# Kernel optimization log

Measured on AMD Instinct MI355X. Metric: run time of the kernel, lower is better.

The kernel has to match this reference:

```python
import jax, jax.numpy as jnp
import numpy as np

B = 16384
F = 1024
DELTA = 0.3
LAMB = 0.0005


def setup_inputs() -> dict:
    key = jax.random.key(0)
    k1, k2, k3, k4 = jax.random.split(key, 4)
    skt = jax.random.normal(k1, (B, F), dtype=jnp.float32)
    imgp = jax.random.normal(k2, (B, F), dtype=jnp.float32)
    imgn = jax.random.normal(k3, (B, F), dtype=jnp.float32)
    eye = jnp.eye(F, dtype=jnp.float32)
    w = eye + 0.05 * jax.random.normal(k4, (F, F), dtype=jnp.float32)
    return {"skt": skt, "imgp": imgp, "imgn": imgn, "w": w, "eye": eye}


def _distance(v1, v2, w, w_rowsum, w_colsum):
    # sum_{i,j} w[i,j] * (v1[:,i] - v2[:,j])**2
    #   = (v1**2) @ w.sum(1) - 2 * v1 @ w @ v2^T (diag) + (v2**2) @ w.sum(0)
    cross = ((v1 @ w) * v2).sum(axis=-1)  # [B]
    return (v1 * v1) @ w_rowsum - 2.0 * cross + (v2 * v2) @ w_colsum


def reference(skt, imgp, imgn, w, eye):
    w_rowsum = w.sum(axis=1)  # [F]
    w_colsum = w.sum(axis=0)  # [F]
    dp = _distance(skt, imgp, w, w_rowsum, w_colsum)  # [B]
    dn = _distance(skt, imgn, w, w_rowsum, w_colsum)  # [B]
    hinge = jnp.maximum(DELTA + dp - dn, 0.0).mean()
    dw = w - eye
    regu = jnp.abs(dw).sum() + jnp.sqrt((dw * dw).sum())
    return hinge + LAMB * regu
```

## Files before the change

kernel.cpp:

```cpp
#include <hip/hip_runtime.h>
#include <hip/hip_bf16.h>

#define FDIM 1024
#define BROWS 16384
#define DELTA_C 0.3f
#define LAMB_C 0.0005f

typedef __bf16 bf8v __attribute__((ext_vector_type(8)));
typedef float f4v __attribute__((ext_vector_type(4)));
typedef unsigned short u16;
typedef u16 u16x8 __attribute__((ext_vector_type(8)));

#define WS_PABS_OFF 4160
#define WS_PSQ_OFF 4672
#define WS_ROWACC_OFF 8192
#define WS_WB_OFF 131072
#define WS_SKTB_OFF (131072 + (1u << 21))
#define WS_NEED_FULL ((size_t)WS_SKTB_OFF + ((size_t)1 << 25))

__device__ __forceinline__ u16 f2bf(float f) {
  unsigned u = __builtin_bit_cast(unsigned, f);
  u += 0x7fffu + ((u >> 16) & 1u);
  return (u16)(u >> 16);
}

__device__ __forceinline__ void gload_lds16(const void* g, void* l) {
  __builtin_amdgcn_global_load_lds(
      (const __attribute__((address_space(1))) unsigned int*)g,
      (__attribute__((address_space(3))) unsigned int*)l, 16, 0, 0);
}

template <bool DO_A>
__global__ __launch_bounds__(256) void prep_all(const float* __restrict__ w,
                                                const float* __restrict__ skt,
                                                float* __restrict__ colsum,
                                                float* __restrict__ pabs,
                                                float* __restrict__ psq,
                                                u16* __restrict__ wb,
                                                u16* __restrict__ sktb) {
  __shared__ char smem_u[17440];
  const int t = threadIdx.x;
  const int bid = blockIdx.x;

  if (bid < 128) {
    u16(*tile)[1024] = (u16(*)[1024])smem_u;
    float* red = (float*)(smem_u + 16384);
    const int b = bid;
    const int k0 = b * 8;
    const int col = t * 4;

    float cs0 = 0.f, cs1 = 0.f, cs2 = 0.f, cs3 = 0.f;
    float aacc = 0.f, sacc = 0.f;
#pragma unroll
    for (int i = 0; i < 8; ++i) {
      const int gk = k0 + i;
      const float4 v = *(const float4*)(w + (size_t)gk * FDIM + col);
      ushort4 bb;
      bb.x = f2bf(v.x); bb.y = f2bf(v.y); bb.z = f2bf(v.z); bb.w = f2bf(v.w);
      *(ushort4*)(&tile[i][col]) = bb;
      cs0 += v.x; cs1 += v.y; cs2 += v.z; cs3 += v.w;
      const float d0 = v.x - (gk == col + 0 ? 1.f : 0.f);
      const float d1 = v.y - (gk == col + 1 ? 1.f : 0.f);
      const float d2 = v.z - (gk == col + 2 ? 1.f : 0.f);
      const float d3 = v.w - (gk == col + 3 ? 1.f : 0.f);
      aacc += fabsf(d0) + fabsf(d1) + fabsf(d2) + fabsf(d3);
      sacc += d0 * d0 + d1 * d1 + d2 * d2 + d3 * d3;
    }
    atomicAdd(&colsum[col + 0], cs0);
    atomicAdd(&colsum[col + 1], cs1);
    atomicAdd(&colsum[col + 2], cs2);
    atomicAdd(&colsum[col + 3], cs3);
#pragma unroll
    for (int off = 1; off < 64; off <<= 1) {
      aacc += __shfl_xor(aacc, off);
      sacc += __shfl_xor(sacc, off);
    }
    const int wid = t >> 6;
    if ((t & 63) == 0) { red[wid] = aacc; red[4 + wid] = sacc; }
    __syncthreads();
    if (t == 0) pabs[b] = red[0] + red[1] + red[2] + red[3];
    if (t == 1) psq[b] = red[4] + red[5] + red[6] + red[7];
#pragma unroll
    for (int j = 0; j < 4; ++j) {
      const int n = col + j;
      u16x8 pk;
#pragma unroll
      for (int e = 0; e < 8; ++e) pk[e] = tile[e][n];
      *(u16x8*)(wb + ((size_t)b * FDIM + n) * 8) = pk;
    }
  } else if constexpr (DO_A) {
    u16(*tile)[136] = (u16(*)[136])smem_u;
    const int ab = bid - 128;
    const int mb = ab >> 3;
    const int kb = ab & 7;
    const int m0 = mb * 64, k0 = kb * 128;
#pragma unroll
    for (int i = 0; i < 8; ++i) {
      const int fid = i * 256 + t;
      const int ml = fid >> 5;
      const int c4 = fid & 31;
      const float4 v = *(const float4*)(skt + (size_t)(m0 + ml) * FDIM + k0 + c4 * 4);
      ushort4 b;
      b.x = f2bf(v.x); b.y = f2bf(v.y); b.z = f2bf(v.z); b.w = f2bf(v.w);
      *(ushort4*)(&tile[ml][c4 * 4]) = b;
    }
    __syncthreads();
    const int ks0 = k0 >> 3;
#pragma unroll
    for (int i = 0; i < 4; ++i) {
      const int uid = i * 256 + t;
      const int si = uid >> 6;
      const int ml = uid & 63;
      const u16x8 pk = *(const u16x8*)(&tile[ml][si * 8]);
      *(u16x8*)(sktb + ((size_t)(ks0 + si) * BROWS + m0 + ml) * 8) = pk;
    }
  }
}

template <bool PRE>
__global__ __launch_bounds__(512, 4) void hofel_main(
    const float* __restrict__ skt, const float* __restrict__ imgp,
    const float* __restrict__ imgn, const u16* __restrict__ wb,
    const u16* __restrict__ sktb, const float* __restrict__ colsum,
    float* __restrict__ rowacc) {
  __shared__ u16 ldsT[3][12288];
  __shared__ float lds_cs[128];

  const int t = threadIdx.x;
  const int lane = t & 63;
  const int wid = t >> 6;
  const int l15 = lane & 15;
  const int l4 = lane >> 4;

  const int swz = (blockIdx.x & 7) * 64 + (blockIdx.x >> 3);
  const int mt = swz >> 3, nt = swz & 7;
  const int m0 = mt * 256, n0 = nt * 128;

  const int wr = wid >> 1, wc = wid & 1;
  const int wm = wr * 64, wn = wc * 64;

  f4v acc[4][4];
#pragma unroll
  for (int mi = 0; mi < 4; ++mi)
#pragma unroll
    for (int ni = 0; ni < 4; ++ni) {
      f4v z = {0.f, 0.f, 0.f, 0.f};
      acc[mi][ni] = z;
    }

  auto stage = [&](int buf, int kt) {
#pragma unroll
    for (int r = 0; r < 2; ++r) {
      const int o = r * 8192 + wid * 1024;
      const int ol = o + lane * 16;
      const int s = ol >> 12;
      const int m = (ol >> 4) & 255;
      gload_lds16((const char*)(sktb + ((size_t)(kt * 4 + s) * BROWS + m0 + m) * 8),
                  (char*)ldsT[buf] + o);
    }
    {
      const int o2 = wid * 1024;
      const int ol2 = o2 + lane * 16;
      const int s = ol2 >> 11;
      const int n = (ol2 >> 4) & 127;
      gload_lds16((const char*)(wb + ((size_t)(kt * 4 + s) * FDIM + n0 + n) * 8),
                  (char*)ldsT[buf] + 16384 + o2);
    }
  };

  auto compute_tile = [&](int buf) {
    const char* bufb = (const char*)ldsT[buf];
    bf8v aF[4], bF[4];
#pragma unroll
    for (int mi = 0; mi < 4; ++mi)
      aF[mi] = *(const bf8v*)(bufb + l4 * 4096 + (wm + mi * 16 + l15) * 16);
#pragma unroll
    for (int ni = 0; ni < 4; ++ni)
      bF[ni] = *(const bf8v*)(bufb + 16384 + l4 * 2048 + (wn + ni * 16 + l15) * 16);
#pragma unroll
    for (int mi = 0; mi < 4; ++mi)
#pragma unroll
      for (int ni = 0; ni < 4; ++ni)
        acc[mi][ni] = __builtin_amdgcn_mfma_f32_16x16x32_bf16(aF[mi], bF[ni], acc[mi][ni], 0, 0, 0);
  };

  if constexpr (PRE) {
    if (t < 128) lds_cs[t] = colsum[n0 + t];
    asm volatile("s_waitcnt vmcnt(0) lgkmcnt(0)" ::: "memory");
    __builtin_amdgcn_sched_barrier(0);
    stage(0, 0);
    stage(1, 1);
    asm volatile("s_waitcnt vmcnt(3)" ::: "memory");
    __builtin_amdgcn_s_barrier();
    __builtin_amdgcn_sched_barrier(0);

    int cur = 0;
    for (int kt = 0; kt < 32; ++kt) {
      if (kt + 2 < 32) {
        const int nb = (cur >= 1) ? cur - 1 : cur + 2;
        stage(nb, kt + 2);
      }
      compute_tile(cur);
      if (kt < 30) {
        asm volatile("s_waitcnt vmcnt(3)" ::: "memory");
        __builtin_amdgcn_s_barrier();
        __builtin_amdgcn_sched_barrier(0);
      } else if (kt == 30) {
        asm volatile("s_waitcnt vmcnt(0)" ::: "memory");
        __builtin_amdgcn_s_barrier();
        __builtin_amdgcn_sched_barrier(0);
      }
      cur = (cur == 2) ? 0 : cur + 1;
    }
  } else {
    if (t < 128) lds_cs[t] = colsum[n0 + t];
    for (int kt = 0; kt < 32; ++kt) {
      __syncthreads();
      {
        const int o2 = wid * 1024;
        const int ol2 = o2 + lane * 16;
        const int s = ol2 >> 11;
        const int n = (ol2 >> 4) & 127;
        gload_lds16((const char*)(wb + ((size_t)(kt * 4 + s) * FDIM + n0 + n) * 8),
                    (char*)ldsT[0] + 16384 + o2);
      }
      const int m = t >> 1, h = t & 1;
      const float* ap = skt + (size_t)(m0 + m) * FDIM + kt * 32 + h * 16;
#pragma unroll
      for (int q = 0; q < 2; ++q) {
        const float4 v0 = *(const float4*)(ap + q * 8);
        const float4 v1 = *(const float4*)(ap + q * 8 + 4);
        u16x8 pk;
        pk[0] = f2bf(v0.x); pk[1] = f2bf(v0.y); pk[2] = f2bf(v0.z); pk[3] = f2bf(v0.w);
        pk[4] = f2bf(v1.x); pk[5] = f2bf(v1.y); pk[6] = f2bf(v1.z); pk[7] = f2bf(v1.w);
        *(u16x8*)((char*)ldsT[0] + (h * 2 + q) * 4096 + m * 16) = pk;
      }
      __syncthreads();
      compute_tile(0);
    }
  }

#pragma unroll
  for (int mi = 0; mi < 4; ++mi) {
#pragma unroll
    for (int rr = 0; rr < 4; ++rr) {
      const int row = m0 + wm + mi * 16 + l4 * 4 + rr;
      const float* pr = imgp + (size_t)row * FDIM + n0;
      const float* nr = imgn + (size_t)row * FDIM + n0;
      float s = 0.f;
#pragma unroll
      for (int ni = 0; ni < 4; ++ni) {
        const int cl = wn + ni * 16 + l15;
        const float T = acc[mi][ni][rr];
        const float p = pr[cl];
        const float q = nr[cl];
        s += (p - q) * (-2.f * T + (p + q) * lds_cs[cl]);
      }
#pragma unroll
      for (int off = 1; off < 16; off <<= 1) s += __shfl_xor(s, off);
      if (l15 == 0) atomicAdd(rowacc + row, s);
    }
  }
}

__global__ __launch_bounds__(1024) void hinge_reduce(const float* __restrict__ rowacc,
                                                     float* __restrict__ wsf) {
  __shared__ float part[16];
  const int t = threadIdx.x;
  const int id = blockIdx.x * 1024 + t;
  float v = fmaxf(DELTA_C + rowacc[id], 0.f);
#pragma unroll
  for (int off = 1; off < 64; off <<= 1) v += __shfl_xor(v, off);
  if ((t & 63) == 0) part[t >> 6] = v;
  __syncthreads();
  if (t < 16) {
    float x = part[t];
#pragma unroll
    for (int off = 1; off < 16; off <<= 1) x += __shfl_xor(x, off);
    if (t == 0) atomicAdd(&wsf[0], x);
  }
}

__global__ __launch_bounds__(128) void finalize_k(const float* __restrict__ wsf,
                                                  const float* __restrict__ pabs,
                                                  const float* __restrict__ psq,
                                                  float* __restrict__ out) {
  __shared__ float ra[2], rs[2];
  const int t = threadIdx.x;
  float a = pabs[t], s = psq[t];
#pragma unroll
  for (int off = 1; off < 64; off <<= 1) {
    a += __shfl_xor(a, off);
    s += __shfl_xor(s, off);
  }
  if ((t & 63) == 0) { ra[t >> 6] = a; rs[t >> 6] = s; }
  __syncthreads();
  if (t == 0)
    out[0] = wsf[0] * (1.f / (float)BROWS) +
             LAMB_C * ((ra[0] + ra[1]) + sqrtf(rs[0] + rs[1]));
}

extern "C" void kernel_launch(void* const* d_in, const int* in_sizes, int n_in,
                              void* d_out, int out_size, void* d_ws, size_t ws_size,
                              hipStream_t stream) {
  const float* skt  = (const float*)d_in[0];
  const float* imgp = (const float*)d_in[1];
  const float* imgn = (const float*)d_in[2];
  const float* w    = (const float*)d_in[3];

  float* wsf = (float*)d_ws;
  float* colsum = wsf + 16;
  float* pabs = (float*)((char*)d_ws + WS_PABS_OFF);
  float* psq = (float*)((char*)d_ws + WS_PSQ_OFF);
  float* rowacc = (float*)((char*)d_ws + WS_ROWACC_OFF);
  u16* wb = (u16*)((char*)d_ws + WS_WB_OFF);
  u16* sktb = (u16*)((char*)d_ws + WS_SKTB_OFF);
  float* out = (float*)d_out;

  hipMemsetAsync(d_ws, 0, WS_ROWACC_OFF + BROWS * sizeof(float), stream);

  if (ws_size >= WS_NEED_FULL) {
    prep_all<true><<<128 + 2048, 256, 0, stream>>>(w, skt, colsum, pabs, psq, wb, sktb);
    hofel_main<true><<<512, 512, 0, stream>>>(skt, imgp, imgn, wb, sktb, colsum, rowacc);
  } else {
    prep_all<false><<<128, 256, 0, stream>>>(w, skt, colsum, pabs, psq, wb, sktb);
    hofel_main<false><<<512, 512, 0, stream>>>(skt, imgp, imgn, wb, sktb, colsum, rowacc);
  }

  hinge_reduce<<<16, 1024, 0, stream>>>(rowacc, wsf);
  finalize_k<<<1, 128, 0, stream>>>(wsf, pabs, psq, out);
}
```

Before: 88.48 us.

## Enlarge GEMM tiles to 256x256 with 4-stage LDS pipeline and priority hints

Each block of the main GEMM now computes a 256x256 output tile instead of 256x128, so the grid halves to 256 blocks, one per CU. Each wave now holds a 128x64 accumulator. The LDS pipeline goes from three to four stages with three loads in flight. The compute is split into two MFMA half-phases around a barrier, wrapped in s_setprio to favour the matrix cores. The skt conversion blocks in the prep kernel are reordered by swizzle. The aim is more data reuse per staged byte and less LDS/global traffic per FLOP, at the cost of higher register pressure (launch bounds lowered to 2) and less occupancy to hide latency.

```diff
diff --git a/kernel.cpp b/kernel.cpp
--- a/kernel.cpp
+++ b/kernel.cpp
@@ -90,7 +90,8 @@
     }
   } else if constexpr (DO_A) {
     u16(*tile)[136] = (u16(*)[136])smem_u;
-    const int ab = bid - 128;
+    const int bidp = bid - 128;
+    const int ab = ((bidp & 7) << 8) | (bidp >> 3);
     const int mb = ab >> 3;
     const int kb = ab & 7;
     const int m0 = mb * 64, k0 = kb * 128;
@@ -117,14 +118,17 @@
   }
 }
 
+#define MM(mi, ni, a, b) \
+  acc[mi][ni] = __builtin_amdgcn_mfma_f32_16x16x32_bf16(a, b, acc[mi][ni], 0, 0, 0)
+
 template <bool PRE>
-__global__ __launch_bounds__(512, 4) void hofel_main(
+__global__ __launch_bounds__(512, 2) void hofel_main(
     const float* __restrict__ skt, const float* __restrict__ imgp,
     const float* __restrict__ imgn, const u16* __restrict__ wb,
     const u16* __restrict__ sktb, const float* __restrict__ colsum,
     float* __restrict__ rowacc) {
-  __shared__ u16 ldsT[3][12288];
-  __shared__ float lds_cs[128];
+  __shared__ u16 ldsT[4][16384];
+  __shared__ float lds_cs[256];
 
   const int t = threadIdx.x;
   const int lane = t & 63;
@@ -132,16 +136,19 @@
   const int l15 = lane & 15;
   const int l4 = lane >> 4;
 
-  const int swz = (blockIdx.x & 7) * 64 + (blockIdx.x >> 3);
-  const int mt = swz >> 3, nt = swz & 7;
-  const int m0 = mt * 256, n0 = nt * 128;
-
-  const int wr = wid >> 1, wc = wid & 1;
-  const int wm = wr * 64, wn = wc * 64;
-
-  f4v acc[4][4];
-#pragma unroll
-  for (int mi = 0; mi < 4; ++mi)
+  const int swz = (blockIdx.x & 7) * 32 + (blockIdx.x >> 3);
+  const int mt = swz >> 2, nt = swz & 3;
+  const int m0 = mt * 256, n0 = nt * 256;
+
+  const int wr = wid >> 2, wc = wid & 3;
+  const int wm = wr * 128, wn = wc * 64;
+
+  const int aoff = l4 * 4096 + (wm + l15) * 16;
+  const int boff = l4 * 4096 + (wn + l15) * 16;
+
+  f4v acc[8][4];
+#pragma unroll
+  for (int mi = 0; mi < 8; ++mi)
 #pragma unroll
     for (int ni = 0; ni < 4; ++ni) {
       f4v z = {0.f, 0.f, 0.f, 0.f};
@@ -158,71 +165,87 @@
       gload_lds16((const char*)(sktb + ((size_t)(kt * 4 + s) * BROWS + m0 + m) * 8),
                   (char*)ldsT[buf] + o);
     }
-    {
-      const int o2 = wid * 1024;
-      const int ol2 = o2 + lane * 16;
-      const int s = ol2 >> 11;
-      const int n = (ol2 >> 4) & 127;
+#pragma unroll
+    for (int r = 0; r < 2; ++r) {
+      const int o = r * 8192 + wid * 1024;
+      const int ol = o + lane * 16;
+      const int s = ol >> 12;
+      const int n = (ol >> 4) & 255;
       gload_lds16((const char*)(wb + ((size_t)(kt * 4 + s) * FDIM + n0 + n) * 8),
-                  (char*)ldsT[buf] + 16384 + o2);
+                  (char*)ldsT[buf] + 16384 + o);
     }
   };
 
-  auto compute_tile = [&](int buf) {
-    const char* bufb = (const char*)ldsT[buf];
-    bf8v aF[4], bF[4];
-#pragma unroll
-    for (int mi = 0; mi < 4; ++mi)
-      aF[mi] = *(const bf8v*)(bufb + l4 * 4096 + (wm + mi * 16 + l15) * 16);
-#pragma unroll
-    for (int ni = 0; ni < 4; ++ni)
-      bF[ni] = *(const bf8v*)(bufb + 16384 + l4 * 2048 + (wn + ni * 16 + l15) * 16);
-#pragma unroll
-    for (int mi = 0; mi < 4; ++mi)
-#pragma unroll
-      for (int ni = 0; ni < 4; ++ni)
-        acc[mi][ni] = __builtin_amdgcn_mfma_f32_16x16x32_bf16(aF[mi], bF[ni], acc[mi][ni], 0, 0, 0);
-  };
-
   if constexpr (PRE) {
-    if (t < 128) lds_cs[t] = colsum[n0 + t];
+    if (t < 256) lds_cs[t] = colsum[n0 + t];
     asm volatile("s_waitcnt vmcnt(0) lgkmcnt(0)" ::: "memory");
     __builtin_amdgcn_sched_barrier(0);
     stage(0, 0);
     stage(1, 1);
-    asm volatile("s_waitcnt vmcnt(3)" ::: "memory");
+    stage(2, 2);
+    asm volatile("s_waitcnt vmcnt(8)" ::: "memory");
     __builtin_amdgcn_s_barrier();
     __builtin_amdgcn_sched_barrier(0);
 
-    int cur = 0;
     for (int kt = 0; kt < 32; ++kt) {
-      if (kt + 2 < 32) {
-        const int nb = (cur >= 1) ? cur - 1 : cur + 2;
-        stage(nb, kt + 2);
-      }
-      compute_tile(cur);
-      if (kt < 30) {
-        asm volatile("s_waitcnt vmcnt(3)" ::: "memory");
-        __builtin_amdgcn_s_barrier();
-        __builtin_amdgcn_sched_barrier(0);
+      const char* ldsA = (const char*)ldsT[kt & 3];
+      const char* ldsB = ldsA + 16384;
+
+      bf8v bF0 = *(const bf8v*)(ldsB + boff);
+      bf8v bF1 = *(const bf8v*)(ldsB + boff + 256);
+      bf8v bF2 = *(const bf8v*)(ldsB + boff + 512);
+      bf8v bF3 = *(const bf8v*)(ldsB + boff + 768);
+      bf8v a0 = *(const bf8v*)(ldsA + aoff);
+      bf8v a1 = *(const bf8v*)(ldsA + aoff + 256);
+      bf8v a2 = *(const bf8v*)(ldsA + aoff + 512);
+      bf8v a3 = *(const bf8v*)(ldsA + aoff + 768);
+      if (kt < 29) stage((kt + 3) & 3, kt + 3);
+      asm volatile("s_waitcnt lgkmcnt(0)" ::: "memory");
+      __builtin_amdgcn_sched_barrier(0);
+      __builtin_amdgcn_s_setprio(1);
+      MM(0, 0, a0, bF0); MM(0, 1, a0, bF1); MM(0, 2, a0, bF2); MM(0, 3, a0, bF3);
+      MM(1, 0, a1, bF0); MM(1, 1, a1, bF1); MM(1, 2, a1, bF2); MM(1, 3, a1, bF3);
+      MM(2, 0, a2, bF0); MM(2, 1, a2, bF1); MM(2, 2, a2, bF2); MM(2, 3, a2, bF3);
+      MM(3, 0, a3, bF0); MM(3, 1, a3, bF1); MM(3, 2, a3, bF2); MM(3, 3, a3, bF3);
+      __builtin_amdgcn_s_setprio(0);
+      __builtin_amdgcn_s_barrier();
+      __builtin_amdgcn_sched_barrier(0);
+
+      a0 = *(const bf8v*)(ldsA + aoff + 1024);
+      a1 = *(const bf8v*)(ldsA + aoff + 1280);
+      a2 = *(const bf8v*)(ldsA + aoff + 1536);
+      a3 = *(const bf8v*)(ldsA + aoff + 1792);
+      asm volatile("s_waitcnt lgkmcnt(0)" ::: "memory");
+      __builtin_amdgcn_sched_barrier(0);
+      __builtin_amdgcn_s_setprio(1);
+      MM(4, 0, a0, bF0); MM(4, 1, a0, bF1); MM(4, 2, a0, bF2); MM(4, 3, a0, bF3);
+      MM(5, 0, a1, bF0); MM(5, 1, a1, bF1); MM(5, 2, a1, bF2); MM(5, 3, a1, bF3);
+      MM(6, 0, a2, bF0); MM(6, 1, a2, bF1); MM(6, 2, a2, bF2); MM(6, 3, a2, bF3);
+      MM(7, 0, a3, bF0); MM(7, 1, a3, bF1); MM(7, 2, a3, bF2); MM(7, 3, a3, bF3);
+      __builtin_amdgcn_s_setprio(0);
+
+      if (kt < 29) {
+        asm volatile("s_waitcnt vmcnt(8)" ::: "memory");
+      } else if (kt == 29) {
+        asm volatile("s_waitcnt vmcnt(4)" ::: "memory");
       } else if (kt == 30) {
         asm volatile("s_waitcnt vmcnt(0)" ::: "memory");
-        __builtin_amdgcn_s_barrier();
-        __builtin_amdgcn_sched_barrier(0);
-      }
-      cur = (cur == 2) ? 0 : cur + 1;
+      }
+      if (kt < 31) __builtin_amdgcn_s_barrier();
+      __builtin_amdgcn_sched_barrier(0);
     }
   } else {
-    if (t < 128) lds_cs[t] = colsum[n0 + t];
+    if (t < 256) lds_cs[t] = colsum[n0 + t];
     for (int kt = 0; kt < 32; ++kt) {
       __syncthreads();
-      {
-        const int o2 = wid * 1024;
-        const int ol2 = o2 + lane * 16;
-        const int s = ol2 >> 11;
-        const int n = (ol2 >> 4) & 127;
+#pragma unroll
+      for (int r = 0; r < 2; ++r) {
+        const int o = r * 8192 + wid * 1024;
+        const int ol = o + lane * 16;
+        const int s = ol >> 12;
+        const int n = (ol >> 4) & 255;
         gload_lds16((const char*)(wb + ((size_t)(kt * 4 + s) * FDIM + n0 + n) * 8),
-                    (char*)ldsT[0] + 16384 + o2);
+                    (char*)ldsT[0] + 16384 + o);
       }
       const int m = t >> 1, h = t & 1;
       const float* ap = skt + (size_t)(m0 + m) * FDIM + kt * 32 + h * 16;
@@ -236,12 +259,28 @@
         *(u16x8*)((char*)ldsT[0] + (h * 2 + q) * 4096 + m * 16) = pk;
       }
       __syncthreads();
-      compute_tile(0);
-    }
-  }
-
-#pragma unroll
-  for (int mi = 0; mi < 4; ++mi) {
+      const char* ldsA = (const char*)ldsT[0];
+      const char* ldsB = ldsA + 16384;
+      bf8v bF0 = *(const bf8v*)(ldsB + boff);
+      bf8v bF1 = *(const bf8v*)(ldsB + boff + 256);
+      bf8v bF2 = *(const bf8v*)(ldsB + boff + 512);
+      bf8v bF3 = *(const bf8v*)(ldsB + boff + 768);
+#pragma unroll
+      for (int mh = 0; mh < 8; mh += 4) {
+        bf8v a0 = *(const bf8v*)(ldsA + aoff + (mh + 0) * 256);
+        bf8v a1 = *(const bf8v*)(ldsA + aoff + (mh + 1) * 256);
+        bf8v a2 = *(const bf8v*)(ldsA + aoff + (mh + 2) * 256);
+        bf8v a3 = *(const bf8v*)(ldsA + aoff + (mh + 3) * 256);
+        MM(mh + 0, 0, a0, bF0); MM(mh + 0, 1, a0, bF1); MM(mh + 0, 2, a0, bF2); MM(mh + 0, 3, a0, bF3);
+        MM(mh + 1, 0, a1, bF0); MM(mh + 1, 1, a1, bF1); MM(mh + 1, 2, a1, bF2); MM(mh + 1, 3, a1, bF3);
+        MM(mh + 2, 0, a2, bF0); MM(mh + 2, 1, a2, bF1); MM(mh + 2, 2, a2, bF2); MM(mh + 2, 3, a2, bF3);
+        MM(mh + 3, 0, a3, bF0); MM(mh + 3, 1, a3, bF1); MM(mh + 3, 2, a3, bF2); MM(mh + 3, 3, a3, bF3);
+      }
+    }
+  }
+
+#pragma unroll
+  for (int mi = 0; mi < 8; ++mi) {
 #pragma unroll
     for (int rr = 0; rr < 4; ++rr) {
       const int row = m0 + wm + mi * 16 + l4 * 4 + rr;
@@ -321,10 +360,10 @@
 
   if (ws_size >= WS_NEED_FULL) {
     prep_all<true><<<128 + 2048, 256, 0, stream>>>(w, skt, colsum, pabs, psq, wb, sktb);
-    hofel_main<true><<<512, 512, 0, stream>>>(skt, imgp, imgn, wb, sktb, colsum, rowacc);
+    hofel_main<true><<<256, 512, 0, stream>>>(skt, imgp, imgn, wb, sktb, colsum, rowacc);
   } else {
     prep_all<false><<<128, 256, 0, stream>>>(w, skt, colsum, pabs, psq, wb, sktb);
-    hofel_main<false><<<512, 512, 0, stream>>>(skt, imgp, imgn, wb, sktb, colsum, rowacc);
+    hofel_main<false><<<256, 512, 0, stream>>>(skt, imgp, imgn, wb, sktb, colsum, rowacc);
   }
 
   hinge_reduce<<<16, 1024, 0, stream>>>(rowacc, wsf);
```

Result: no change. 90.15 us (+1.9%).
